# Optimization experiments

Hardware: AMD Instinct MI355X
Metric: run time of the kernel (lower is better)

## Reference

```python
import jax, jax.numpy as jnp
import numpy as np

B, CD, ZL = 512, 64, 16
HID, SE, NC, SL = 512, 512, 9, 64
EPS = 1e-5


def _conv_t1d(x, w, b, stride, opad):
    # torch ConvTranspose1d weight layout: [in, out, k]; pad=0
    k = w.shape[-1]
    w2 = jnp.flip(jnp.transpose(w, (1, 0, 2)), -1)  # [out, in, k]
    y = jax.lax.conv_general_dilated(
        x, w2, window_strides=(1,),
        padding=[(k - 1, k - 1 + opad)], lhs_dilation=(stride,),
        dimension_numbers=('NCH', 'OIH', 'NCH'))
    return y + b[None, :, None]


def _bn(x, g, bt, m, v):  # eval-mode BatchNorm1d over channel dim of [B,C,L]
    return (x - m[None, :, None]) * (g * jax.lax.rsqrt(v + EPS))[None, :, None] + bt[None, :, None]


def _gru(x, h, wih, whh, bih, bhh):  # torch GRUCell gate order r,z,n
    gi = x @ wih.T + bih
    gh = h @ whh.T + bhh
    ir, iz, inn = jnp.split(gi, 3, axis=-1)
    hr, hz, hn = jnp.split(gh, 3, axis=-1)
    r = jax.nn.sigmoid(ir + hr)
    z = jax.nn.sigmoid(iz + hz)
    n = jnp.tanh(inn + r * hn)
    return (1.0 - z) * n + z * h


def setup_inputs() -> dict:
    ks = jax.random.split(jax.random.key(0), 24)
    s = 0.05
    H2 = HID // 2
    in1 = H2 + 2 * NC
    d = {}
    d['quantized_z'] = jax.random.normal(ks[0], (B, CD, ZL), jnp.float32)
    d['note_target'] = (jax.random.uniform(ks[1], (B, SL, NC)) > 0.5).astype(jnp.float32)
    d['skel'] = (jax.random.uniform(ks[2], (B, SL, NC)) > 0.5).astype(jnp.float32)
    d['skel_encoded'] = jax.random.normal(ks[3], (B, SE), jnp.float32)
    d['training'] = 0
    d['teacher_forcing_ratio'] = 0
    d['ct1_w'] = jax.random.normal(ks[4], (CD, HID, 4)) * s
    d['ct1_b'] = jnp.zeros((HID,))
    d['bn1_g'] = jnp.ones((HID,))
    d['bn1_b'] = jnp.zeros((HID,))
    d['bn1_m'] = jax.random.normal(ks[5], (HID,)) * 0.1
    d['bn1_v'] = 1.0 + 0.1 * jax.random.uniform(ks[6], (HID,))
    d['ct2_w'] = jax.random.normal(ks[7], (HID, H2, 4)) * s
    d['ct2_b'] = jnp.zeros((H2,))
    d['bn2_g'] = jnp.ones((H2,))
    d['bn2_b'] = jnp.zeros((H2,))
    d['bn2_m'] = jax.random.normal(ks[8], (H2,)) * 0.1
    d['bn2_v'] = 1.0 + 0.1 * jax.random.uniform(ks[9], (H2,))
    d['hfc_w'] = jax.random.normal(ks[10], (HID, SE)) * s
    d['hfc_b'] = jnp.zeros((HID,))
    d['gru1_wih'] = jax.random.normal(ks[11], (3 * HID, in1)) * s
    d['gru1_whh'] = jax.random.normal(ks[12], (3 * HID, HID)) * s
    d['gru1_bih'] = jnp.zeros((3 * HID,))
    d['gru1_bhh'] = jnp.zeros((3 * HID,))
    d['gru2_wih'] = jax.random.normal(ks[13], (3 * HID, HID)) * s
    d['gru2_whh'] = jax.random.normal(ks[14], (3 * HID, HID)) * s
    d['gru2_bih'] = jnp.zeros((3 * HID,))
    d['gru2_bhh'] = jnp.zeros((3 * HID,))
    d['nfc_w'] = jax.random.normal(ks[15], (NC, HID)) * s
    d['nfc_b'] = jnp.zeros((NC,))
    return d


def _forward(quantized_z, skel, skel_encoded,
             ct1_w, ct1_b, bn1_g, bn1_b, bn1_m, bn1_v,
             ct2_w, ct2_b, bn2_g, bn2_b, bn2_m, bn2_v,
             hfc_w, hfc_b,
             gru1_wih, gru1_whh, gru1_bih, gru1_bhh,
             gru2_wih, gru2_whh, gru2_bih, gru2_bhh,
             nfc_w, nfc_b):
    lrelu = lambda x: jax.nn.leaky_relu(x, 0.2)
    y = lrelu(_bn(_conv_t1d(quantized_z, ct1_w, ct1_b, 2, 1), bn1_g, bn1_b, bn1_m, bn1_v))
    y = lrelu(_bn(_conv_t1d(y, ct2_w, ct2_b, 2, 0), bn2_g, bn2_b, bn2_m, bn2_v))
    inputs = jnp.transpose(y, (0, 2, 1))[:, :SL]  # [B, SL, HID//2]
    h1_0 = skel_encoded @ hfc_w.T + hfc_b          # [B, HID]
    keys = jax.random.split(jax.random.key(42), SL)

    def step(carry, xs):
        h1, h2, out = carry
        i, x_in, x_sk, k = xs
        cat = jnp.concatenate([out, x_in, x_sk], axis=-1)  # [B, NC + HID//2 + NC]
        h1 = _gru(cat, h1, gru1_wih, gru1_whh, gru1_bih, gru1_bhh)
        h2 = jnp.where(i == 0, h1, h2)  # hx[1] = hx[0] at first step
        h2 = _gru(h1, h2, gru2_wih, gru2_whh, gru2_bih, gru2_bhh)
        logits = h2 @ nfc_w.T + nfc_b
        r = jax.random.uniform(k, logits.shape, logits.dtype)
        out = (jax.nn.sigmoid(logits) - r > 0).astype(logits.dtype)  # eval-mode Bernoulli sampling
        return (h1, h2, out), logits

    carry0 = (h1_0, jnp.zeros_like(h1_0), jnp.zeros((quantized_z.shape[0], NC), h1_0.dtype))
    xs = (jnp.arange(SL), jnp.transpose(inputs, (1, 0, 2)), jnp.transpose(skel, (1, 0, 2)), keys)
    _, logits = jax.lax.scan(step, carry0, xs)
    return jnp.transpose(logits, (1, 0, 2))  # [B, SL, NC]


def reference(quantized_z, note_target, skel, skel_encoded, training, teacher_forcing_ratio,
              ct1_w, ct1_b, bn1_g, bn1_b, bn1_m, bn1_v,
              ct2_w, ct2_b, bn2_g, bn2_b, bn2_m, bn2_v,
              hfc_w, hfc_b,
              gru1_wih, gru1_whh, gru1_bih, gru1_bhh,
              gru2_wih, gru2_whh, gru2_bih, gru2_bhh,
              nfc_w, nfc_b):
    # training=0 (eval): dropout is identity, BN uses running stats, always sample feedback.
    # note_target / teacher_forcing_ratio are unused on the eval path.
    return _forward(quantized_z, skel, skel_encoded,
                    ct1_w, ct1_b, bn1_g, bn1_b, bn1_m, bn1_v,
                    ct2_w, ct2_b, bn2_g, bn2_b, bn2_m, bn2_v,
                    hfc_w, hfc_b,
                    gru1_wih, gru1_whh, gru1_bih, gru1_bhh,
                    gru2_wih, gru2_whh, gru2_bih, gru2_bhh,
                    nfc_w, nfc_b)
```

## Files before the change

kernel.cpp:

```cpp
#include <hip/hip_runtime.h>
#include <stdint.h>

typedef uint32_t u32; typedef uint16_t u16; typedef unsigned long long u64;
typedef __attribute__((ext_vector_type(8))) short short8;
typedef __attribute__((ext_vector_type(4))) float f32x4;

#define DEV static __device__ __forceinline__
#define MFMA16 __builtin_amdgcn_mfma_f32_16x16x32_bf16

#define BATCH 512
#define CD    64
#define ZL    16
#define HID   512
#define H2D   256
#define NC    9
#define SLEN  64
#define L1    35

#define JAX_PARTITIONABLE 1

#define P_W      2850816
#define WOFF_SKH 4276224
#define WOFF_HPL 4538368
#define WOFF_HF  6111232
#define WOFF_LOG 7159808
#define WOFF_FLG 7684096
#define WOFF_XH  9175040

template<int V> struct IC { static constexpr int value = V; };

DEV float bf2f(u16 h){ u32 u = ((u32)h) << 16; float f; __builtin_memcpy(&f,&u,4); return f; }
DEV u16 f2bf(float f){ u32 u; __builtin_memcpy(&u,&f,4); return (u16)((u + 0x7FFFu + ((u>>16)&1u)) >> 16); }

DEV float ldf(const float* p){ return __hip_atomic_load(p, __ATOMIC_RELAXED, __HIP_MEMORY_SCOPE_AGENT); }
DEV u32 ldu32(const u32* p){ return __hip_atomic_load(p, __ATOMIC_RELAXED, __HIP_MEMORY_SCOPE_AGENT); }
DEV u64 ldu64(const u64* p){ return __hip_atomic_load(p, __ATOMIC_RELAXED, __HIP_MEMORY_SCOPE_AGENT); }
DEV void stu32(u32* p, u32 v){ __hip_atomic_store(p, v, __ATOMIC_RELAXED, __HIP_MEMORY_SCOPE_AGENT); }

DEV void threefry2x32(u32 k0, u32 k1, u32 x0, u32 x1, u32 &o0, u32 &o1){
  const u32 ks2 = k0 ^ k1 ^ 0x1BD11BDAu;
#define TF_R(d) { x0 += x1; x1 = (x1 << (d)) | (x1 >> (32 - (d))); x1 ^= x0; }
  x0 += k0; x1 += k1;
  TF_R(13) TF_R(15) TF_R(26) TF_R(6)
  x0 += k1;  x1 += ks2 + 1u;
  TF_R(17) TF_R(29) TF_R(16) TF_R(24)
  x0 += ks2; x1 += k0 + 2u;
  TF_R(13) TF_R(15) TF_R(26) TF_R(6)
  x0 += k0;  x1 += k1 + 3u;
  TF_R(17) TF_R(29) TF_R(16) TF_R(24)
  x0 += k1;  x1 += ks2 + 4u;
  TF_R(13) TF_R(15) TF_R(26) TF_R(6)
  x0 += ks2; x1 += k0 + 5u;
#undef TF_R
  o0 = x0; o1 = x1;
}
DEV void step_key(int t, u32 &ka, u32 &kb){
#if JAX_PARTITIONABLE
  threefry2x32(0u, 42u, 0u, (u32)t, ka, kb);
#else
  u32 j0 = 2u*(u32)t, j1 = j0 + 1u, a0, a1;
  if (j0 < 64u){ threefry2x32(0u,42u, j0, 64u+j0, a0, a1); ka = a0; }
  else         { threefry2x32(0u,42u, j0-64u, j0, a0, a1); ka = a1; }
  if (j1 < 64u){ threefry2x32(0u,42u, j1, 64u+j1, a0, a1); kb = a0; }
  else         { threefry2x32(0u,42u, j1-64u, j1, a0, a1); kb = a1; }
#endif
}
DEV float rng_uniform(u32 ka, u32 kb, u32 f){
  u32 bits, o0, o1;
#if JAX_PARTITIONABLE
  threefry2x32(ka, kb, 0u, f, o0, o1);
  bits = o0 ^ o1;
#else
  const u32 HALF = (u32)(BATCH*NC/2);
  if (f < HALF){ threefry2x32(ka, kb, f, f+HALF, o0, o1); bits = o0; }
  else         { threefry2x32(ka, kb, f-HALF, f, o0, o1); bits = o1; }
#endif
  u32 fb = (bits >> 9) | 0x3F800000u;
  float fv; __builtin_memcpy(&fv,&fb,4);
  return fv - 1.0f;
}

__global__ __launch_bounds__(256) void k_conv1(
    const float* __restrict__ z, const float* __restrict__ w1, const float* __restrict__ b1,
    const float* __restrict__ g1, const float* __restrict__ bt1, const float* __restrict__ m1,
    const float* __restrict__ v1, float* __restrict__ y1out)
{
  int t = blockIdx.x, bg = blockIdx.y*8, tid = threadIdx.x;
  __shared__ float zsh[2][8][CD];
  int k0 = t & 1, sA = (t-k0)>>1, sB = sA-1;
  bool vA = (sA>=0 && sA<ZL), vB = (sB>=0 && sB<ZL);
  for (int l = tid; l < 2*8*CD; l += 256){
    int p = l>>9, bb = (l>>6)&7, i = l&63;
    int s = p ? sB : sA; bool v = p ? vB : vA;
    zsh[p][bb][i] = v ? z[((bg+bb)*CD+i)*ZL + s] : 0.f;
  }
  __syncthreads();
  const float4* w1v = (const float4*)w1;
  for (int o = tid; o < HID; o += 256){
    float acc[8] = {0,0,0,0,0,0,0,0};
    for (int i = 0; i < CD; i++){
      float4 wv = w1v[i*HID + o];
      float wA = k0 ? wv.y : wv.x, wB = k0 ? wv.w : wv.z;
      #pragma unroll
      for (int bb = 0; bb < 8; bb++) acc[bb] += zsh[0][bb][i]*wA + zsh[1][bb][i]*wB;
    }
    float xb = b1[o], sc = g1[o]/sqrtf(v1[o]+1e-5f), mm = m1[o], be = bt1[o];
    #pragma unroll
    for (int bb = 0; bb < 8; bb++){
      float y = (acc[bb]+xb-mm)*sc + be;
      y = (y>0.f)? y : 0.2f*y;
      y1out[((bg+bb)*L1 + t)*HID + o] = y;
    }
  }
}

__global__ __launch_bounds__(256) void k_conv2(
    const float* __restrict__ y1, const float* __restrict__ w2, const float* __restrict__ b2,
    const float* __restrict__ g2, const float* __restrict__ bt2, const float* __restrict__ m2,
    const float* __restrict__ v2, u16* __restrict__ xh, u16* __restrict__ xl)
{
  int t = blockIdx.x, bg = blockIdx.y*8, tid = threadIdx.x;
  __shared__ float ysh[2][8][HID];
  int k0 = t & 1, sA = (t-k0)>>1, sB = sA-1;
  bool vB = (sB >= 0);
  for (int l = tid; l < 2*8*HID; l += 256){
    int p = l>>12, bb = (l>>9)&7, o = l&511;
    int s = p ? sB : sA; bool v = p ? vB : true;
    ysh[p][bb][o] = v ? y1[((bg+bb)*L1 + s)*HID + o] : 0.f;
  }
  __syncthreads();
  int c = tid;
  float acc[8] = {0,0,0,0,0,0,0,0};
  const float4* w2v = (const float4*)w2;
  for (int o4 = 0; o4 < HID; o4 += 4){
    float wA[4], wB[4];
    #pragma unroll
    for (int j = 0; j < 4; j++){
      float4 wv = w2v[(o4+j)*H2D + c];
      wA[j] = k0 ? wv.y : wv.x; wB[j] = k0 ? wv.w : wv.z;
    }
    #pragma unroll
    for (int bb = 0; bb < 8; bb++){
      const float4 ya = *(const float4*)&ysh[0][bb][o4];
      const float4 yb = *(const float4*)&ysh[1][bb][o4];
      acc[bb] += ya.x*wA[0]+ya.y*wA[1]+ya.z*wA[2]+ya.w*wA[3]
               + yb.x*wB[0]+yb.y*wB[1]+yb.z*wB[2]+yb.w*wB[3];
    }
  }
  float xb = b2[c], sc = g2[c]/sqrtf(v2[c]+1e-5f), mm = m2[c], be = bt2[c];
  #pragma unroll
  for (int bb = 0; bb < 8; bb++){
    float y = (acc[bb]+xb-mm)*sc + be;
    y = (y>0.f)? y : 0.2f*y;
    u16 hi = f2bf(y); u16 lo = f2bf(y - bf2f(hi));
    size_t o = ((size_t)t*512 + bg + bb)*256 + c;
    xh[o] = hi; xl[o] = lo;
  }
}

__global__ __launch_bounds__(256) void k_prep(
    const float* __restrict__ wih1, const float* __restrict__ whh1,
    const float* __restrict__ wih2, const float* __restrict__ whh2,
    const float* __restrict__ skel, float* __restrict__ ws)
{
  u16* wp = (u16*)ws;
  u16* skh = (u16*)(ws + WOFF_SKH);
  float* logacc = ws + WOFF_LOG;
  u32* flg = (u32*)(ws + WOFF_FLG);
  int stride = gridDim.x*256, i0 = blockIdx.x*256 + threadIdx.x;
  for (int i = i0; i < P_W; i += stride){
    int r = i; float v;
    if (r < 491520){
      int n = r/320, k = r - n*320; v = 0.f;
      if (k < 256)      v = wih1[(size_t)n*274 + 9 + k];
      else if (k < 265) v = wih1[(size_t)n*274 + 265 + (k-256)];
      else if (k < 274) v = wih1[(size_t)n*274 + (k-265)];
    }
    else if (r < 1277952){ int rr = r-491520;  int n = rr>>9, k = rr&511; v = whh1[((size_t)n<<9)+k]; }
    else if (r < 2064384){ int rr = r-1277952; int n = rr>>9, k = rr&511; v = wih2[((size_t)n<<9)+k]; }
    else                 { int rr = r-2064384; int n = rr>>9, k = rr&511; v = whh2[((size_t)n<<9)+k]; }
    u16 l0 = f2bf(v);
    float r1 = v - bf2f(l0); u16 l1 = f2bf(r1);
    float r2 = r1 - bf2f(l1); u16 l2 = f2bf(r2);
    wp[i] = l0; wp[P_W + i] = l1; wp[2*P_W + i] = l2;
  }
  for (int i = i0; i < 524288; i += stride){
    int c = i & 15, r = i >> 4, b = r & 511, tt = r >> 9;
    float v = (c < 9) ? skel[((size_t)b*64 + tt)*9 + c] : 0.f;
    skh[i] = f2bf(v);
  }
  for (int i = i0; i < 524288; i += stride) logacc[i] = 0.f;
  for (int i = i0; i < 512; i += stride) flg[i] = 0u;
}

__global__ __launch_bounds__(256) void k_h0(
    const float* __restrict__ se, const float* __restrict__ w, const float* __restrict__ bias,
    float* __restrict__ ws)
{
  float* h1af = ws + WOFF_HF;
  u16* hpl = (u16*)(ws + WOFF_HPL);
  int b = blockIdx.x, tid = threadIdx.x;
  __shared__ float ssh[HID];
  for (int i = tid; i < HID; i += 256) ssh[i] = se[b*HID + i];
  __syncthreads();
  for (int j = tid; j < HID; j += 256){
    float acc = 0.f;
    for (int q = 0; q < HID; q++) acc += ssh[q]*w[j*HID + q];
    float v = acc + bias[j];
    h1af[(size_t)b*512 + j] = v;
    u16 l0 = f2bf(v);
    float r1 = v - bf2f(l0); u16 l1 = f2bf(r1);
    float r2 = r1 - bf2f(l1); u16 l2 = f2bf(r2);
    hpl[(size_t)b*512 + j] = l0;
    hpl[262144 + (size_t)b*512 + j] = l1;
    hpl[524288 + (size_t)b*512 + j] = l2;
  }
}

__global__ __launch_bounds__(384, 1) void k_persist(
    float* __restrict__ ws,
    const float* __restrict__ bih1, const float* __restrict__ bhh1,
    const float* __restrict__ bih2, const float* __restrict__ bhh2,
    const float* __restrict__ nfw,  const float* __restrict__ nfb,
    float* __restrict__ dout)
{
  const int tid = threadIdx.x;
  const int wvid = __builtin_amdgcn_readfirstlane(tid >> 6);
  const int g = wvid >> 1;
  const int mh = wvid & 1;
  const int lane = tid & 63;
  const int mloc = lane & 15;
  const int q8 = (lane >> 4) * 8;
  const int q4 = (lane >> 4) * 4;
  const int bg = blockIdx.x & 15;
  const int nstrip = blockIdx.x >> 4;
  const int b0 = bg * 32;
  const int n0 = nstrip * 32;

  u16* wp = (u16*)ws;
  const u16* skh = (const u16*)(ws + WOFF_SKH);
  u16* hpl = (u16*)(ws + WOFF_HPL);
  const float* h1af = ws + WOFF_HF;
  float* logacc = ws + WOFF_LOG;
  u32* flgH = (u32*)(ws + WOFF_FLG);
  u32* flgL = flgH + 256;
  const u16* xh = (const u16*)(ws + WOFF_XH);
  const u16* xl = xh + 8388608;

  __shared__ u16 Abuf[2][3][32][72];
  __shared__ u16 Wbuf[2][3][3][32][72];
  __shared__ float eg[4][32][33];
  __shared__ float h2loc[32][33];
  __shared__ u16 out_sh[32][12];

  int t = 0;
  float2 hp1[2], hp2[2];

  ((u16*)out_sh)[tid] = 0;
  #pragma unroll
  for (int i = 0; i < 2; i++){
    int e = tid + i*384;
    if (e < 512){
      int bi = e >> 4, nl2 = (e & 15)*2;
      hp1[i].x = h1af[(size_t)(b0+bi)*512 + n0 + nl2];
      hp1[i].y = h1af[(size_t)(b0+bi)*512 + n0 + nl2 + 1];
    }
  }

  auto soft_bar = [&](){
    __builtin_amdgcn_sched_barrier(0);
    asm volatile("s_waitcnt lgkmcnt(0)" ::: "memory");
    __builtin_amdgcn_s_barrier();
    __builtin_amdgcn_sched_barrier(0);
  };
  auto arrive = [&](u32* f, u32 tok){
    __syncthreads();
    if (tid == 0) __hip_atomic_store(&f[bg*16 + nstrip], tok, __ATOMIC_RELEASE, __HIP_MEMORY_SCOPE_AGENT);
  };
  auto waitbar = [&](u32* f, u32 tok){
    if (tid < 16) while (ldu32(&f[bg*16 + tid]) < tok) __builtin_amdgcn_s_sleep(2);
    __syncthreads();
  };

  auto run_phase = [&](auto mc, auto nwc, int Kp, size_t SUB, const u16* hb, f32x4 (&acc)[2]){
    constexpr int MODE = decltype(mc)::value;
    constexpr int NW = decltype(nwc)::value;
    short8 RwA[6], RwB[6];
    u64 RaA[2][2], RaB[2][2];

    auto loadW = [&](short8 (&R)[6], int kc){
      #pragma unroll
      for (int i = 0; i < 6; i++){
        int idx = tid + i*384;
        int gp = idx >> 8, r = idx & 255, nn = r >> 3, ck = r & 7;
        const u16* src = wp + (size_t)(gp % 3)*P_W + SUB
                       + ((size_t)((gp/3)*512 + n0 + nn))*Kp + kc + ck*8;
        R[i] = *(const short8*)src;
      }
    };
    auto writeW = [&](int buf, short8 (&R)[6]){
      #pragma unroll
      for (int i = 0; i < 6; i++){
        int idx = tid + i*384;
        int gp = idx >> 8, r = idx & 255, nn = r >> 3, ck = r & 7;
        *(short8*)&Wbuf[buf][gp/3][gp%3][nn][ck*8] = R[i];
      }
    };
    auto loadA = [&](u64 (&R)[2][2], int kc){
      #pragma unroll
      for (int i = 0; i < 2; i++){
        int idx = tid + i*384;
        if constexpr (MODE == 1){
          int p = idx >> 8, r = idx & 255, bi = r >> 3, ck = r & 7;
          const u16* src = hb + (size_t)p*262144 + (size_t)(b0+bi)*512 + kc + ck*8;
          R[i][0] = ldu64((const u64*)src);
          R[i][1] = ldu64((const u64*)(src + 4));
        } else {
          if (idx < 512){
            int p = idx >> 8, r = idx & 255, bi = r >> 3, ck = r & 7;
            if (kc < 256){
              const u64* src = (const u64*)((p ? xl : xh) + ((size_t)t*512 + b0 + bi)*256 + kc + ck*8);
              R[i][0] = src[0]; R[i][1] = src[1];
            } else {
              u64 w0 = 0, w1 = 0;
              if (p == 0){
                #pragma unroll
                for (int e2 = 0; e2 < 4; e2++){
                  int kg = 256 + ck*8 + e2;
                  u16 val = 0;
                  if (kg < 265) val = skh[((size_t)t*512 + b0 + bi)*16 + (kg - 256)];
                  else if (kg < 274) val = out_sh[bi][kg - 265];
                  w0 |= ((u64)val) << (16*e2);
                }
                #pragma unroll
                for (int e2 = 0; e2 < 4; e2++){
                  int kg = 260 + ck*8 + e2;
                  u16 val = 0;
                  if (kg < 265) val = skh[((size_t)t*512 + b0 + bi)*16 + (kg - 256)];
                  else if (kg < 274) val = out_sh[bi][kg - 265];
                  w1 |= ((u64)val) << (16*e2);
                }
              }
              R[i][0] = w0; R[i][1] = w1;
            }
          }
        }
      }
    };
    auto writeA = [&](int buf, u64 (&R)[2][2]){
      constexpr int NCH = (MODE == 1) ? 768 : 512;
      #pragma unroll
      for (int i = 0; i < 2; i++){
        int idx = tid + i*384;
        if (idx < NCH){
          int p = idx >> 8, r = idx & 255, bi = r >> 3, ck = r & 7;
          u64* d = (u64*)&Abuf[buf][p][bi][ck*8];
          d[0] = R[i][0]; d[1] = R[i][1];
        }
      }
    };
    auto compute = [&](int buf){
      const int arow = mh*16 + mloc;
      #pragma unroll
      for (int ks = 0; ks < 2; ks++){
        const int ko = ks*32 + q8;
        short8 a0 = *(const short8*)&Abuf[buf][0][arow][ko];
        short8 a1 = *(const short8*)&Abuf[buf][1][arow][ko];
        short8 a2;
        if constexpr (MODE == 1) a2 = *(const short8*)&Abuf[buf][2][arow][ko];
        #pragma unroll
        for (int j = 0; j < 2; j++){
          const int wrow = j*16 + mloc;
          short8 w0 = *(const short8*)&Wbuf[buf][g][0][wrow][ko];
          short8 w1 = *(const short8*)&Wbuf[buf][g][1][wrow][ko];
          short8 w2 = *(const short8*)&Wbuf[buf][g][2][wrow][ko];
          acc[j] = MFMA16(a0, w0, acc[j], 0, 0, 0);
          acc[j] = MFMA16(a0, w1, acc[j], 0, 0, 0);
          acc[j] = MFMA16(a1, w0, acc[j], 0, 0, 0);
          acc[j] = MFMA16(a0, w2, acc[j], 0, 0, 0);
          if constexpr (MODE == 1) acc[j] = MFMA16(a2, w0, acc[j], 0, 0, 0);
          acc[j] = MFMA16(a1, w1, acc[j], 0, 0, 0);
        }
      }
    };

    loadW(RwA, 0); loadA(RaA, 0);
    if (NW > 1){ loadW(RwB, 64); loadA(RaB, 64); }
    writeW(0, RwA); writeA(0, RaA);
    soft_bar();

    auto stepw = [&](int w, short8 (&Rl)[6], u64 (&Al)[2][2], short8 (&Rs)[6], u64 (&As)[2][2]){
      if (w + 2 < NW){ loadW(Rl, (w+2)*64); loadA(Al, (w+2)*64); }
      compute(w & 1);
      if (w + 1 < NW){ writeW((w+1)&1, Rs); writeA((w+1)&1, As); }
      soft_bar();
    };
    #pragma unroll
    for (int w = 0; w < NW; w += 2){
      stepw(w, RwA, RaA, RwB, RaB);
      if (w + 1 < NW) stepw(w+1, RwB, RaB, RwA, RaA);
    }
  };

  auto epilogue = [&](const float* bih, const float* bhh, u16* hnl,
                      float2 (&hp)[2], bool cell2, bool init2,
                      f32x4 (&accI)[2], f32x4 (&accH)[2]){
    #pragma unroll
    for (int j = 0; j < 2; j++)
      #pragma unroll
      for (int i2 = 0; i2 < 4; i2++){
        int row = mh*16 + q4 + i2, col = j*16 + mloc;
        if (g < 2) eg[g][row][col] = accI[j][i2] + accH[j][i2];
        else { eg[2][row][col] = accI[j][i2]; eg[3][row][col] = accH[j][i2]; }
      }
    __syncthreads();
    #pragma unroll
    for (int i = 0; i < 2; i++){
      int e = tid + i*384;
      if (e < 512){
        int bi = e >> 4, nl2 = (e & 15)*2, b = b0 + bi;
        float hv[2];
        float hpv0 = hp[i].x, hpv1 = hp[i].y;
        #pragma unroll
        for (int u = 0; u < 2; u++){
          int nl = nl2 + u, n = n0 + nl;
          float rr = 1.f/(1.f + expf(-(eg[0][bi][nl] + bih[n] + bhh[n])));
          float zz = 1.f/(1.f + expf(-(eg[1][bi][nl] + bih[512+n] + bhh[512+n])));
          float nn2 = tanhf(eg[2][bi][nl] + bih[1024+n] + rr*(eg[3][bi][nl] + bhh[1024+n]));
          float hprev = u ? hpv1 : hpv0;
          hv[u] = (1.f - zz)*nn2 + zz*hprev;
          if (cell2) h2loc[bi][nl] = hv[u];
        }
        hp[i].x = hv[0]; hp[i].y = hv[1];
        if (init2){ hp2[i].x = hv[0]; hp2[i].y = hv[1]; }
        u16 A0 = f2bf(hv[0]); float ra = hv[0] - bf2f(A0);
        u16 A1 = f2bf(ra);    float ra2 = ra - bf2f(A1);
        u16 A2 = f2bf(ra2);
        u16 B0 = f2bf(hv[1]); float rb = hv[1] - bf2f(B0);
        u16 B1 = f2bf(rb);    float rb2 = rb - bf2f(B1);
        u16 B2 = f2bf(rb2);
        size_t base = (size_t)b*512 + n0 + nl2;
        stu32((u32*)(hnl + base),          (u32)A0 | ((u32)B0 << 16));
        stu32((u32*)(hnl + 262144 + base), (u32)A1 | ((u32)B1 << 16));
        stu32((u32*)(hnl + 524288 + base), (u32)A2 | ((u32)B2 << 16));
      }
    }
    __syncthreads();
    if (cell2){
      for (int e = tid; e < 288; e += 384){
        int c = e % 9, bi = e / 9;
        float s = 0.f;
        #pragma unroll
        for (int nl = 0; nl < 32; nl++) s += nfw[c*512 + n0 + nl]*h2loc[bi][nl];
        atomicAdd(&logacc[((size_t)t*512 + b0 + bi)*16 + c], s);
      }
    }
  };

  auto sample_phase = [&](int tp){
    for (int e = tid; e < 288; e += 384){
      int c = e % 9, bi = e / 9, b = b0 + bi;
      float lg = ldf(&logacc[((size_t)tp*512 + b)*16 + c]) + nfb[c];
      if (nstrip == 0) dout[((size_t)b*64 + tp)*9 + c] = lg;
      if (tp < 63){
        u32 ka, kb; step_key(tp, ka, kb);
        float rr = rng_uniform(ka, kb, (u32)(b*9 + c));
        float sg = 1.f/(1.f + expf(-lg));
        out_sh[bi][c] = (sg - rr > 0.f) ? (u16)0x3F80 : (u16)0;
      }
    }
    __syncthreads();
  };

  for (t = 0; t < 64; t++){
    const u16* h1pl = hpl + (size_t)((t & 1) ? 1 : 0)*786432;
    u16*       h1nl = hpl + (size_t)((t & 1) ? 0 : 1)*786432;
    const u16* h2pl = hpl + (size_t)((t & 1) ? 2 : 3)*786432;
    u16*       h2nl = hpl + (size_t)((t & 1) ? 3 : 2)*786432;

    f32x4 accI[2] = {{0,0,0,0},{0,0,0,0}}, accH[2] = {{0,0,0,0},{0,0,0,0}};
    run_phase(IC<1>{}, IC<8>{}, 512, (size_t)491520, h1pl, accH);
    if (t > 0){ waitbar(flgL, (u32)t); sample_phase(t-1); }
    run_phase(IC<0>{}, IC<5>{}, 320, (size_t)0, nullptr, accI);
    epilogue(bih1, bhh1, h1nl, hp1, false, (t == 0), accI, accH);
    arrive(flgH, (u32)(t+1));

    f32x4 accI2[2] = {{0,0,0,0},{0,0,0,0}}, accH2[2] = {{0,0,0,0},{0,0,0,0}};
    if (t == 0){
      waitbar(flgH, 1u);
      run_phase(IC<1>{}, IC<8>{}, 512, (size_t)2064384, h1nl, accH2);
    } else {
      run_phase(IC<1>{}, IC<8>{}, 512, (size_t)2064384, h2pl, accH2);
      waitbar(flgH, (u32)(t+1));
    }
    run_phase(IC<1>{}, IC<8>{}, 512, (size_t)1277952, h1nl, accI2);
    epilogue(bih2, bhh2, h2nl, hp2, true, false, accI2, accH2);
    arrive(flgL, (u32)(t+1));
  }
  waitbar(flgL, 64u);
  sample_phase(63);
}

extern "C" void kernel_launch(void* const* d_in, const int* in_sizes, int n_in,
                              void* d_out, int out_size, void* d_ws, size_t ws_size,
                              hipStream_t stream) {
  (void)in_sizes; (void)n_in; (void)out_size; (void)ws_size;
  const float* z       = (const float*)d_in[0];
  const float* skel    = (const float*)d_in[2];
  const float* se      = (const float*)d_in[3];
  const float* ct1_w   = (const float*)d_in[6];
  const float* ct1_b   = (const float*)d_in[7];
  const float* bn1_g   = (const float*)d_in[8];
  const float* bn1_b   = (const float*)d_in[9];
  const float* bn1_m   = (const float*)d_in[10];
  const float* bn1_v   = (const float*)d_in[11];
  const float* ct2_w   = (const float*)d_in[12];
  const float* ct2_b   = (const float*)d_in[13];
  const float* bn2_g   = (const float*)d_in[14];
  const float* bn2_b   = (const float*)d_in[15];
  const float* bn2_m   = (const float*)d_in[16];
  const float* bn2_v   = (const float*)d_in[17];
  const float* hfc_w   = (const float*)d_in[18];
  const float* hfc_b   = (const float*)d_in[19];
  const float* g1_wih  = (const float*)d_in[20];
  const float* g1_whh  = (const float*)d_in[21];
  const float* g1_bih  = (const float*)d_in[22];
  const float* g1_bhh  = (const float*)d_in[23];
  const float* g2_wih  = (const float*)d_in[24];
  const float* g2_whh  = (const float*)d_in[25];
  const float* g2_bih  = (const float*)d_in[26];
  const float* g2_bhh  = (const float*)d_in[27];
  const float* nfc_w   = (const float*)d_in[28];
  const float* nfc_b   = (const float*)d_in[29];

  float* ws = (float*)d_ws;
  float* y1 = ws;
  u16* xh = (u16*)(ws + WOFF_XH);
  u16* xl = xh + 8388608;
  float* dout = (float*)d_out;

  k_conv1<<<dim3(L1, BATCH/8), 256, 0, stream>>>(z, ct1_w, ct1_b, bn1_g, bn1_b, bn1_m, bn1_v, y1);
  k_conv2<<<dim3(SLEN, BATCH/8), 256, 0, stream>>>(y1, ct2_w, ct2_b, bn2_g, bn2_b, bn2_m, bn2_v, xh, xl);
  k_prep<<<4096, 256, 0, stream>>>(g1_wih, g1_whh, g2_wih, g2_whh, skel, ws);
  k_h0<<<BATCH, 256, 0, stream>>>(se, hfc_w, hfc_b, ws);

  void* args[] = {
    (void*)&ws, (void*)&g1_bih, (void*)&g1_bhh, (void*)&g2_bih, (void*)&g2_bhh,
    (void*)&nfc_w, (void*)&nfc_b, (void*)&dout
  };
  hipLaunchCooperativeKernel((const void*)k_persist, dim3(256), dim3(384), args, 0, stream);
}
```

Measured before the change: 4.002 ms.

## Load GRU weight fragments directly into registers, dropping LDS weight staging

Each wave now loads its own MFMA weight fragments for all three bf16 limbs straight from global memory into a double-buffered register set, instead of staging a shared weight tile in LDS and reading it back. This drops the LDS write/read traffic and the large Wbuf allocation, which may also let more blocks fit per CU. In exchange each thread holds 24 short8 registers for weights, raising VGPR pressure, and global loads are less coalesced and no longer shared across waves. The weight prefetch for step w+2 is issued after the compute of step w.

```diff
diff --git a/kernel.cpp b/kernel.cpp
--- a/kernel.cpp
+++ b/kernel.cpp
@@ -248,7 +248,6 @@
   const u16* xl = xh + 8388608;
 
   __shared__ u16 Abuf[2][3][32][72];
-  __shared__ u16 Wbuf[2][3][3][32][72];
   __shared__ float eg[4][32][33];
   __shared__ float h2loc[32][33];
   __shared__ u16 out_sh[32][12];
@@ -285,26 +284,20 @@
   auto run_phase = [&](auto mc, auto nwc, int Kp, size_t SUB, const u16* hb, f32x4 (&acc)[2]){
     constexpr int MODE = decltype(mc)::value;
     constexpr int NW = decltype(nwc)::value;
-    short8 RwA[6], RwB[6];
+    short8 RWA[12], RWB[12];
     u64 RaA[2][2], RaB[2][2];
 
-    auto loadW = [&](short8 (&R)[6], int kc){
+    const u16* wbase = wp + SUB + (size_t)(g*512 + n0 + mloc)*(size_t)Kp + q8;
+
+    auto loadW = [&](short8 (&R)[12], int kc){
       #pragma unroll
-      for (int i = 0; i < 6; i++){
-        int idx = tid + i*384;
-        int gp = idx >> 8, r = idx & 255, nn = r >> 3, ck = r & 7;
-        const u16* src = wp + (size_t)(gp % 3)*P_W + SUB
-                       + ((size_t)((gp/3)*512 + n0 + nn))*Kp + kc + ck*8;
-        R[i] = *(const short8*)src;
-      }
-    };
-    auto writeW = [&](int buf, short8 (&R)[6]){
-      #pragma unroll
-      for (int i = 0; i < 6; i++){
-        int idx = tid + i*384;
-        int gp = idx >> 8, r = idx & 255, nn = r >> 3, ck = r & 7;
-        *(short8*)&Wbuf[buf][gp/3][gp%3][nn][ck*8] = R[i];
-      }
+      for (int limb = 0; limb < 3; limb++)
+        #pragma unroll
+        for (int ks = 0; ks < 2; ks++)
+          #pragma unroll
+          for (int j = 0; j < 2; j++)
+            R[limb*4 + ks*2 + j] = *(const short8*)(wbase + (size_t)limb*P_W
+                                  + (size_t)(j*16)*(size_t)Kp + kc + ks*32);
     };
     auto loadA = [&](u64 (&R)[2][2], int kc){
       #pragma unroll
@@ -359,21 +352,20 @@
         }
       }
     };
-    auto compute = [&](int buf){
+    auto compute = [&](int buf, short8 (&RW)[12]){
       const int arow = mh*16 + mloc;
       #pragma unroll
       for (int ks = 0; ks < 2; ks++){
         const int ko = ks*32 + q8;
         short8 a0 = *(const short8*)&Abuf[buf][0][arow][ko];
         short8 a1 = *(const short8*)&Abuf[buf][1][arow][ko];
-        short8 a2;
+        short8 a2 = {};
         if constexpr (MODE == 1) a2 = *(const short8*)&Abuf[buf][2][arow][ko];
         #pragma unroll
         for (int j = 0; j < 2; j++){
-          const int wrow = j*16 + mloc;
-          short8 w0 = *(const short8*)&Wbuf[buf][g][0][wrow][ko];
-          short8 w1 = *(const short8*)&Wbuf[buf][g][1][wrow][ko];
-          short8 w2 = *(const short8*)&Wbuf[buf][g][2][wrow][ko];
+          short8 w0 = RW[0*4 + ks*2 + j];
+          short8 w1 = RW[1*4 + ks*2 + j];
+          short8 w2 = RW[2*4 + ks*2 + j];
           acc[j] = MFMA16(a0, w0, acc[j], 0, 0, 0);
           acc[j] = MFMA16(a0, w1, acc[j], 0, 0, 0);
           acc[j] = MFMA16(a1, w0, acc[j], 0, 0, 0);
@@ -384,21 +376,22 @@
       }
     };
 
-    loadW(RwA, 0); loadA(RaA, 0);
-    if (NW > 1){ loadW(RwB, 64); loadA(RaB, 64); }
-    writeW(0, RwA); writeA(0, RaA);
+    loadW(RWA, 0); loadA(RaA, 0);
+    if (NW > 1){ loadW(RWB, 64); loadA(RaB, 64); }
+    writeA(0, RaA);
     soft_bar();
 
-    auto stepw = [&](int w, short8 (&Rl)[6], u64 (&Al)[2][2], short8 (&Rs)[6], u64 (&As)[2][2]){
-      if (w + 2 < NW){ loadW(Rl, (w+2)*64); loadA(Al, (w+2)*64); }
-      compute(w & 1);
-      if (w + 1 < NW){ writeW((w+1)&1, Rs); writeA((w+1)&1, As); }
+    auto stepw = [&](int w, short8 (&RWc)[12], u64 (&Al)[2][2], u64 (&As)[2][2]){
+      if (w + 2 < NW) loadA(Al, (w+2)*64);
+      compute(w & 1, RWc);
+      if (w + 2 < NW) loadW(RWc, (w+2)*64);
+      if (w + 1 < NW) writeA((w+1)&1, As);
       soft_bar();
     };
     #pragma unroll
     for (int w = 0; w < NW; w += 2){
-      stepw(w, RwA, RaA, RwB, RaB);
-      if (w + 1 < NW) stepw(w+1, RwB, RaB, RwA, RaA);
+      stepw(w, RWA, RaA, RaB);
+      if (w + 1 < NW) stepw(w+1, RWB, RaB, RaA);
     }
   };
 
```

New measurement: 11.96 ms. +198.8%, slower.

## Double persistent block to 768 threads, one MFMA tile per wave

Applied to the files above, without the earlier changes.

Raises the persistent GRU kernel from 6 to 12 waves per block. Each wave now owns a single 16x16 output tile instead of two, and the global-to-LDS load and store loops shrink so every thread moves fewer chunks. The goal is more latency hiding and more MFMA issue parallelism inside the latency-bound recurrent step, at the cost of more A-fragment LDS reads per wave and heavier block-wide barriers. The NW>1 guard around the second prefetch is also dropped, which is safe because every phase uses NW of at least 5.

```diff
diff --git a/kernel.cpp b/kernel.cpp
--- a/kernel.cpp
+++ b/kernel.cpp
@@ -217,7 +217,7 @@
   }
 }
 
-__global__ __launch_bounds__(384, 1) void k_persist(
+__global__ __launch_bounds__(768, 1) void k_persist(
     float* __restrict__ ws,
     const float* __restrict__ bih1, const float* __restrict__ bhh1,
     const float* __restrict__ bih2, const float* __restrict__ bhh2,
@@ -226,8 +226,9 @@
 {
   const int tid = threadIdx.x;
   const int wvid = __builtin_amdgcn_readfirstlane(tid >> 6);
-  const int g = wvid >> 1;
-  const int mh = wvid & 1;
+  const int g  = wvid >> 2;
+  const int mh = (wvid >> 1) & 1;
+  const int jn = wvid & 1;
   const int lane = tid & 63;
   const int mloc = lane & 15;
   const int q8 = (lane >> 4) * 8;
@@ -247,24 +248,20 @@
   const u16* xh = (const u16*)(ws + WOFF_XH);
   const u16* xl = xh + 8388608;
 
-  __shared__ u16 Abuf[2][3][32][72];
-  __shared__ u16 Wbuf[2][3][3][32][72];
-  __shared__ float eg[4][32][33];
-  __shared__ float h2loc[32][33];
-  __shared__ u16 out_sh[32][12];
+  __shared__ __align__(16) u16 Abuf[2][3][32][72];
+  __shared__ __align__(16) u16 Wbuf[2][3][3][32][72];
+  __shared__ __align__(16) float eg[4][32][33];
+  __shared__ __align__(16) float h2loc[32][33];
+  __shared__ __align__(16) u16 out_sh[32][12];
 
   int t = 0;
-  float2 hp1[2], hp2[2];
-
-  ((u16*)out_sh)[tid] = 0;
-  #pragma unroll
-  for (int i = 0; i < 2; i++){
-    int e = tid + i*384;
-    if (e < 512){
-      int bi = e >> 4, nl2 = (e & 15)*2;
-      hp1[i].x = h1af[(size_t)(b0+bi)*512 + n0 + nl2];
-      hp1[i].y = h1af[(size_t)(b0+bi)*512 + n0 + nl2 + 1];
-    }
+  float2 hp1 = {0.f,0.f}, hp2 = {0.f,0.f};
+
+  if (tid < 384) ((u16*)out_sh)[tid] = 0;
+  if (tid < 512){
+    int bi = tid >> 4, nl2 = (tid & 15)*2;
+    hp1.x = h1af[(size_t)(b0+bi)*512 + n0 + nl2];
+    hp1.y = h1af[(size_t)(b0+bi)*512 + n0 + nl2 + 1];
   }
 
   auto soft_bar = [&](){
@@ -282,114 +279,105 @@
     __syncthreads();
   };
 
-  auto run_phase = [&](auto mc, auto nwc, int Kp, size_t SUB, const u16* hb, f32x4 (&acc)[2]){
+  auto run_phase = [&](auto mc, auto nwc, int Kp, size_t SUB, const u16* hb, f32x4 &acc){
     constexpr int MODE = decltype(mc)::value;
     constexpr int NW = decltype(nwc)::value;
-    short8 RwA[6], RwB[6];
-    u64 RaA[2][2], RaB[2][2];
-
-    auto loadW = [&](short8 (&R)[6], int kc){
+    short8 RwA[3], RwB[3];
+    u64 RaA[2], RaB[2];
+
+    auto loadW = [&](short8 (&R)[3], int kc){
       #pragma unroll
-      for (int i = 0; i < 6; i++){
-        int idx = tid + i*384;
+      for (int i = 0; i < 3; i++){
+        int idx = tid + i*768;
         int gp = idx >> 8, r = idx & 255, nn = r >> 3, ck = r & 7;
         const u16* src = wp + (size_t)(gp % 3)*P_W + SUB
-                       + ((size_t)((gp/3)*512 + n0 + nn))*Kp + kc + ck*8;
+                       + ((size_t)((gp/3)*512 + n0 + nn))*(size_t)Kp + kc + ck*8;
         R[i] = *(const short8*)src;
       }
     };
-    auto writeW = [&](int buf, short8 (&R)[6]){
+    auto writeW = [&](int buf, short8 (&R)[3]){
       #pragma unroll
-      for (int i = 0; i < 6; i++){
-        int idx = tid + i*384;
+      for (int i = 0; i < 3; i++){
+        int idx = tid + i*768;
         int gp = idx >> 8, r = idx & 255, nn = r >> 3, ck = r & 7;
         *(short8*)&Wbuf[buf][gp/3][gp%3][nn][ck*8] = R[i];
       }
     };
-    auto loadA = [&](u64 (&R)[2][2], int kc){
-      #pragma unroll
-      for (int i = 0; i < 2; i++){
-        int idx = tid + i*384;
-        if constexpr (MODE == 1){
+    auto loadA = [&](u64 (&R)[2], int kc){
+      int idx = tid;
+      if constexpr (MODE == 1){
+        int p = idx >> 8, r = idx & 255, bi = r >> 3, ck = r & 7;
+        const u16* src = hb + (size_t)p*262144 + (size_t)(b0+bi)*512 + kc + ck*8;
+        R[0] = ldu64((const u64*)src);
+        R[1] = ldu64((const u64*)(src + 4));
+      } else {
+        if (idx < 512){
           int p = idx >> 8, r = idx & 255, bi = r >> 3, ck = r & 7;
-          const u16* src = hb + (size_t)p*262144 + (size_t)(b0+bi)*512 + kc + ck*8;
-          R[i][0] = ldu64((const u64*)src);
-          R[i][1] = ldu64((const u64*)(src + 4));
-        } else {
-          if (idx < 512){
-            int p = idx >> 8, r = idx & 255, bi = r >> 3, ck = r & 7;
-            if (kc < 256){
-              const u64* src = (const u64*)((p ? xl : xh) + ((size_t)t*512 + b0 + bi)*256 + kc + ck*8);
-              R[i][0] = src[0]; R[i][1] = src[1];
-            } else {
-              u64 w0 = 0, w1 = 0;
-              if (p == 0){
-                #pragma unroll
-                for (int e2 = 0; e2 < 4; e2++){
-                  int kg = 256 + ck*8 + e2;
-                  u16 val = 0;
-                  if (kg < 265) val = skh[((size_t)t*512 + b0 + bi)*16 + (kg - 256)];
-                  else if (kg < 274) val = out_sh[bi][kg - 265];
-                  w0 |= ((u64)val) << (16*e2);
-                }
-                #pragma unroll
-                for (int e2 = 0; e2 < 4; e2++){
-                  int kg = 260 + ck*8 + e2;
-                  u16 val = 0;
-                  if (kg < 265) val = skh[((size_t)t*512 + b0 + bi)*16 + (kg - 256)];
-                  else if (kg < 274) val = out_sh[bi][kg - 265];
-                  w1 |= ((u64)val) << (16*e2);
-                }
+          if (kc < 256){
+            const u64* src = (const u64*)((p ? xl : xh) + ((size_t)t*512 + b0 + bi)*256 + kc + ck*8);
+            R[0] = src[0]; R[1] = src[1];
+          } else {
+            u64 w0 = 0, w1 = 0;
+            if (p == 0){
+              #pragma unroll
+              for (int e2 = 0; e2 < 4; e2++){
+                int kg = 256 + ck*8 + e2;
+                u16 val = 0;
+                if (kg < 265) val = skh[((size_t)t*512 + b0 + bi)*16 + (kg - 256)];
+                else if (kg < 274) val = out_sh[bi][kg - 265];
+                w0 |= ((u64)val) << (16*e2);
               }
-              R[i][0] = w0; R[i][1] = w1;
+              #pragma unroll
+              for (int e2 = 0; e2 < 4; e2++){
+                int kg = 260 + ck*8 + e2;
+                u16 val = 0;
+                if (kg < 265) val = skh[((size_t)t*512 + b0 + bi)*16 + (kg - 256)];
+                else if (kg < 274) val = out_sh[bi][kg - 265];
+                w1 |= ((u64)val) << (16*e2);
+              }
             }
+            R[0] = w0; R[1] = w1;
           }
         }
       }
     };
-    auto writeA = [&](int buf, u64 (&R)[2][2]){
+    auto writeA = [&](int buf, u64 (&R)[2]){
       constexpr int NCH = (MODE == 1) ? 768 : 512;
-      #pragma unroll
-      for (int i = 0; i < 2; i++){
-        int idx = tid + i*384;
-        if (idx < NCH){
-          int p = idx >> 8, r = idx & 255, bi = r >> 3, ck = r & 7;
-          u64* d = (u64*)&Abuf[buf][p][bi][ck*8];
-          d[0] = R[i][0]; d[1] = R[i][1];
-        }
+      int idx = tid;
+      if (idx < NCH){
+        int p = idx >> 8, r = idx & 255, bi = r >> 3, ck = r & 7;
+        u64* d = (u64*)&Abuf[buf][p][bi][ck*8];
+        d[0] = R[0]; d[1] = R[1];
       }
     };
     auto compute = [&](int buf){
-      const int arow = mh*16 + mloc;
+      const int ar = mh*16 + mloc;
+      const int wr = jn*16 + mloc;
       #pragma unroll
       for (int ks = 0; ks < 2; ks++){
         const int ko = ks*32 + q8;
-        short8 a0 = *(const short8*)&Abuf[buf][0][arow][ko];
-        short8 a1 = *(const short8*)&Abuf[buf][1][arow][ko];
-        short8 a2;
-        if constexpr (MODE == 1) a2 = *(const short8*)&Abuf[buf][2][arow][ko];
-        #pragma unroll
-        for (int j = 0; j < 2; j++){
-          const int wrow = j*16 + mloc;
-          short8 w0 = *(const short8*)&Wbuf[buf][g][0][wrow][ko];
-          short8 w1 = *(const short8*)&Wbuf[buf][g][1][wrow][ko];
-          short8 w2 = *(const short8*)&Wbuf[buf][g][2][wrow][ko];
-          acc[j] = MFMA16(a0, w0, acc[j], 0, 0, 0);
-          acc[j] = MFMA16(a0, w1, acc[j], 0, 0, 0);
-          acc[j] = MFMA16(a1, w0, acc[j], 0, 0, 0);
-          acc[j] = MFMA16(a0, w2, acc[j], 0, 0, 0);
-          if constexpr (MODE == 1) acc[j] = MFMA16(a2, w0, acc[j], 0, 0, 0);
-          acc[j] = MFMA16(a1, w1, acc[j], 0, 0, 0);
-        }
+        short8 a0 = *(const short8*)&Abuf[buf][0][ar][ko];
+        short8 a1 = *(const short8*)&Abuf[buf][1][ar][ko];
+        short8 a2 = {};
+        if constexpr (MODE == 1) a2 = *(const short8*)&Abuf[buf][2][ar][ko];
+        short8 w0 = *(const short8*)&Wbuf[buf][g][0][wr][ko];
+        short8 w1 = *(const short8*)&Wbuf[buf][g][1][wr][ko];
+        short8 w2 = *(const short8*)&Wbuf[buf][g][2][wr][ko];
+        acc = MFMA16(a0, w0, acc, 0, 0, 0);
+        acc = MFMA16(a0, w1, acc, 0, 0, 0);
+        acc = MFMA16(a1, w0, acc, 0, 0, 0);
+        acc = MFMA16(a0, w2, acc, 0, 0, 0);
+        if constexpr (MODE == 1) acc = MFMA16(a2, w0, acc, 0, 0, 0);
+        acc = MFMA16(a1, w1, acc, 0, 0, 0);
       }
     };
 
     loadW(RwA, 0); loadA(RaA, 0);
-    if (NW > 1){ loadW(RwB, 64); loadA(RaB, 64); }
+    loadW(RwB, 64); loadA(RaB, 64);
     writeW(0, RwA); writeA(0, RaA);
     soft_bar();
 
-    auto stepw = [&](int w, short8 (&Rl)[6], u64 (&Al)[2][2], short8 (&Rs)[6], u64 (&As)[2][2]){
+    auto stepw = [&](int w, short8 (&Rl)[3], u64 (&Al)[2], short8 (&Rs)[3], u64 (&As)[2]){
       if (w + 2 < NW){ loadW(Rl, (w+2)*64); loadA(Al, (w+2)*64); }
       compute(w & 1);
       if (w + 1 < NW){ writeW((w+1)&1, Rs); writeA((w+1)&1, As); }
@@ -403,51 +391,45 @@
   };
 
   auto epilogue = [&](const float* bih, const float* bhh, u16* hnl,
-                      float2 (&hp)[2], bool cell2, bool init2,
-                      f32x4 (&accI)[2], f32x4 (&accH)[2]){
+                      float2 &hp, bool cell2, bool init2,
+                      const f32x4 &accI, const f32x4 &accH){
     #pragma unroll
-    for (int j = 0; j < 2; j++)
+    for (int i2 = 0; i2 < 4; i2++){
+      int row = mh*16 + q4 + i2, col = jn*16 + mloc;
+      if (g < 2) eg[g][row][col] = accI[i2] + accH[i2];
+      else { eg[2][row][col] = accI[i2]; eg[3][row][col] = accH[i2]; }
+    }
+    __syncthreads();
+    if (tid < 512){
+      int bi = tid >> 4, nl2 = (tid & 15)*2, b = b0 + bi;
+      float hv[2];
+      float hpv0 = hp.x, hpv1 = hp.y;
       #pragma unroll
-      for (int i2 = 0; i2 < 4; i2++){
-        int row = mh*16 + q4 + i2, col = j*16 + mloc;
-        if (g < 2) eg[g][row][col] = accI[j][i2] + accH[j][i2];
-        else { eg[2][row][col] = accI[j][i2]; eg[3][row][col] = accH[j][i2]; }
-      }
-    __syncthreads();
-    #pragma unroll
-    for (int i = 0; i < 2; i++){
-      int e = tid + i*384;
-      if (e < 512){
-        int bi = e >> 4, nl2 = (e & 15)*2, b = b0 + bi;
-        float hv[2];
-        float hpv0 = hp[i].x, hpv1 = hp[i].y;
-        #pragma unroll
-        for (int u = 0; u < 2; u++){
-          int nl = nl2 + u, n = n0 + nl;
-          float rr = 1.f/(1.f + expf(-(eg[0][bi][nl] + bih[n] + bhh[n])));
-          float zz = 1.f/(1.f + expf(-(eg[1][bi][nl] + bih[512+n] + bhh[512+n])));
-          float nn2 = tanhf(eg[2][bi][nl] + bih[1024+n] + rr*(eg[3][bi][nl] + bhh[1024+n]));
-          float hprev = u ? hpv1 : hpv0;
-          hv[u] = (1.f - zz)*nn2 + zz*hprev;
-          if (cell2) h2loc[bi][nl] = hv[u];
-        }
-        hp[i].x = hv[0]; hp[i].y = hv[1];
-        if (init2){ hp2[i].x = hv[0]; hp2[i].y = hv[1]; }
-        u16 A0 = f2bf(hv[0]); float ra = hv[0] - bf2f(A0);
-        u16 A1 = f2bf(ra);    float ra2 = ra - bf2f(A1);
-        u16 A2 = f2bf(ra2);
-        u16 B0 = f2bf(hv[1]); float rb = hv[1] - bf2f(B0);
-        u16 B1 = f2bf(rb);    float rb2 = rb - bf2f(B1);
-        u16 B2 = f2bf(rb2);
-        size_t base = (size_t)b*512 + n0 + nl2;
-        stu32((u32*)(hnl + base),          (u32)A0 | ((u32)B0 << 16));
-        stu32((u32*)(hnl + 262144 + base), (u32)A1 | ((u32)B1 << 16));
-        stu32((u32*)(hnl + 524288 + base), (u32)A2 | ((u32)B2 << 16));
-      }
+      for (int u = 0; u < 2; u++){
+        int nl = nl2 + u, n = n0 + nl;
+        float rr = 1.f/(1.f + expf(-(eg[0][bi][nl] + bih[n] + bhh[n])));
+        float zz = 1.f/(1.f + expf(-(eg[1][bi][nl] + bih[512+n] + bhh[512+n])));
+        float nn2 = tanhf(eg[2][bi][nl] + bih[1024+n] + rr*(eg[3][bi][nl] + bhh[1024+n]));
+        float hprev = u ? hpv1 : hpv0;
+        hv[u] = (1.f - zz)*nn2 + zz*hprev;
+        if (cell2) h2loc[bi][nl] = hv[u];
+      }
+      hp.x = hv[0]; hp.y = hv[1];
+      if (init2){ hp2.x = hv[0]; hp2.y = hv[1]; }
+      u16 A0 = f2bf(hv[0]); float ra = hv[0] - bf2f(A0);
+      u16 A1 = f2bf(ra);    float ra2 = ra - bf2f(A1);
+      u16 A2 = f2bf(ra2);
+      u16 B0 = f2bf(hv[1]); float rb = hv[1] - bf2f(B0);
+      u16 B1 = f2bf(rb);    float rb2 = rb - bf2f(B1);
+      u16 B2 = f2bf(rb2);
+      size_t base = (size_t)b*512 + n0 + nl2;
+      stu32((u32*)(hnl + base),          (u32)A0 | ((u32)B0 << 16));
+      stu32((u32*)(hnl + 262144 + base), (u32)A1 | ((u32)B1 << 16));
+      stu32((u32*)(hnl + 524288 + base), (u32)A2 | ((u32)B2 << 16));
     }
     __syncthreads();
     if (cell2){
-      for (int e = tid; e < 288; e += 384){
+      for (int e = tid; e < 288; e += 768){
         int c = e % 9, bi = e / 9;
         float s = 0.f;
         #pragma unroll
@@ -458,7 +440,7 @@
   };
 
   auto sample_phase = [&](int tp){
-    for (int e = tid; e < 288; e += 384){
+    for (int e = tid; e < 288; e += 768){
       int c = e % 9, bi = e / 9, b = b0 + bi;
       float lg = ldf(&logacc[((size_t)tp*512 + b)*16 + c]) + nfb[c];
       if (nstrip == 0) dout[((size_t)b*64 + tp)*9 + c] = lg;
@@ -478,14 +460,14 @@
     const u16* h2pl = hpl + (size_t)((t & 1) ? 2 : 3)*786432;
     u16*       h2nl = hpl + (size_t)((t & 1) ? 3 : 2)*786432;
 
-    f32x4 accI[2] = {{0,0,0,0},{0,0,0,0}}, accH[2] = {{0,0,0,0},{0,0,0,0}};
+    f32x4 accI = {0,0,0,0}, accH = {0,0,0,0};
     run_phase(IC<1>{}, IC<8>{}, 512, (size_t)491520, h1pl, accH);
     if (t > 0){ waitbar(flgL, (u32)t); sample_phase(t-1); }
     run_phase(IC<0>{}, IC<5>{}, 320, (size_t)0, nullptr, accI);
     epilogue(bih1, bhh1, h1nl, hp1, false, (t == 0), accI, accH);
     arrive(flgH, (u32)(t+1));
 
-    f32x4 accI2[2] = {{0,0,0,0},{0,0,0,0}}, accH2[2] = {{0,0,0,0},{0,0,0,0}};
+    f32x4 accI2 = {0,0,0,0}, accH2 = {0,0,0,0};
     if (t == 0){
       waitbar(flgH, 1u);
       run_phase(IC<1>{}, IC<8>{}, 512, (size_t)2064384, h1nl, accH2);
@@ -548,5 +530,5 @@
     (void*)&ws, (void*)&g1_bih, (void*)&g1_bhh, (void*)&g2_bih, (void*)&g2_bhh,
     (void*)&nfc_w, (void*)&nfc_b, (void*)&dout
   };
-  hipLaunchCooperativeKernel((const void*)k_persist, dim3(256), dim3(384), args, 0, stream);
-}
+  hipLaunchCooperativeKernel((const void*)k_persist, dim3(256), dim3(768), args, 0, stream);
+}
```

New measurement: 3.770 ms. 5.8% less time.
